# Performance work log

Hardware: AMD Instinct MI355X
Metric: run time of the kernel (lower is better)

The kernel has to match this reference:

```python
import jax, jax.numpy as jnp
import numpy as np

R_MAX, S_MAX, C_Z = 32, 2, 128
N_POS = 2 * (R_MAX + 1)   # 66 one-hot bins for rel position / rel token
N_CH = 2 * (S_MAX + 1)    # 6 one-hot bins for rel chain
IN_DIM = 2 * N_POS + 1 + N_CH  # 139
B, N = 1, 1024


def setup_inputs() -> dict:
    key = jax.random.key(0)
    k1, k2, k3, k4, k5 = jax.random.split(key, 5)
    asym_id = jnp.sort(jax.random.randint(k1, (B, N), 0, 4), axis=-1)
    residue_index = jnp.sort(jax.random.randint(k2, (B, N), 0, 800), axis=-1)
    entity_id = jnp.sort(jax.random.randint(k3, (B, N), 0, 3), axis=-1)
    sym_id = jax.random.randint(k4, (B, N), 0, 4)
    token_index = jnp.arange(B * N, dtype=jnp.int64 if jax.config.read('jax_enable_x64') else jnp.int32).reshape(B, N)
    W = jax.random.normal(k5, (IN_DIM, C_Z), dtype=jnp.float32)  # transposed LinearNoBias weight
    return {"asym_id": asym_id, "residue_index": residue_index, "entity_id": entity_id,
            "sym_id": sym_id, "token_index": token_index, "W": W}


def reference(asym_id, residue_index, entity_id, sym_id, token_index, W):
    # Pairwise comparisons, [B, N, N]
    same_chain = asym_id[..., :, None] == asym_id[..., None, :]
    same_res = residue_index[..., :, None] == residue_index[..., None, :]
    same_ent = entity_id[..., :, None] == entity_id[..., None, :]

    d_res = jnp.clip(residue_index[..., :, None] - residue_index[..., None, :] + R_MAX, 0, 2 * R_MAX)
    d_res = jnp.where(same_chain, d_res, 2 * R_MAX + 1)

    d_tok = jnp.clip(token_index[..., :, None] - token_index[..., None, :] + R_MAX, 0, 2 * R_MAX)
    d_tok = jnp.where(same_chain & same_res, d_tok, 2 * R_MAX + 1)

    d_chain = jnp.clip(sym_id[..., :, None] - sym_id[..., None, :] + S_MAX, 0, 2 * S_MAX)
    d_chain = jnp.where(same_ent, d_chain, 2 * S_MAX + 1)

    # one_hot(idx) @ W  ==  W[idx]; concat+linear == sum of gathered rows.
    W_pos = W[:N_POS]                     # rows for a_rel_pos
    W_tok = W[N_POS:2 * N_POS]            # rows for a_rel_token
    w_ent = W[2 * N_POS]                  # single row scaled by same_entity flag
    W_ch = W[2 * N_POS + 1:]              # rows for a_rel_chain

    p = (W_pos[d_res] + W_tok[d_tok]
         + same_ent[..., None].astype(W.dtype) * w_ent
         + W_ch[d_chain])                 # [B, N, N, c_z]
    return p
```

## Files before the change

kernel.cpp:

```cpp
#include <hip/hip_runtime.h>


#define RMAX 32
#define SMAX 2
#define CZ 128
#define TJ 512
#define NROWS 138
#define BLOCK 256

__global__ __launch_bounds__(BLOCK) void relpos_kernel(
    const int* __restrict__ asym, const int* __restrict__ resi,
    const int* __restrict__ ent,  const int* __restrict__ sym,
    const int* __restrict__ tok,  const float* __restrict__ W,
    float* __restrict__ out, int N)
{
    __shared__ float4 sW4[NROWS * 32];
    __shared__ int2   sOff[TJ];

    const int tid = threadIdx.x;
    const int i   = blockIdx.y;
    const int j0  = blockIdx.x * TJ;

    const float4* __restrict__ W4 = reinterpret_cast<const float4*>(W);

    for (int t = tid; t < NROWS * 32; t += BLOCK) {
        const int row = t >> 5, cc = t & 31;
        float4 a, b;
        if (row < 66) {
            a = W4[32 * 32 + cc];
            b = W4[(66 + row) * 32 + cc];
        } else if (row < 132) {
            a = W4[(row - 66) * 32 + cc];
            b = W4[131 * 32 + cc];
        } else if (row < 137) {
            a = W4[(133 + (row - 132)) * 32 + cc];
            b = W4[132 * 32 + cc];
        } else {
            a = W4[138 * 32 + cc];
            b = make_float4(0.f, 0.f, 0.f, 0.f);
        }
        sW4[t] = make_float4(a.x + b.x, a.y + b.y, a.z + b.z, a.w + b.w);
    }

    const int ai = asym[i], ri = resi[i], ei = ent[i], si = sym[i], ti = tok[i];
    for (int t = tid; t < TJ; t += BLOCK) {
        const int j = j0 + t;
        const int aj = asym[j], rj = resi[j], ej = ent[j], sj = sym[j], tj = tok[j];
        int row;
        if (ai == aj) {
            if (ri == rj) {
                int dt = ti - tj + RMAX;
                dt = dt < 0 ? 0 : (dt > 2 * RMAX ? 2 * RMAX : dt);
                row = dt;
            } else {
                int dr = ri - rj + RMAX;
                dr = dr < 0 ? 0 : (dr > 2 * RMAX ? 2 * RMAX : dr);
                row = 66 + dr;
            }
        } else {
            row = 131;
        }
        int crow;
        if (ei == ej) {
            int dc = si - sj + SMAX;
            dc = dc < 0 ? 0 : (dc > 2 * SMAX ? 2 * SMAX : dc);
            crow = 132 + dc;
        } else {
            crow = 137;
        }
        sOff[t] = make_int2(row << 5, crow << 5);
    }
    __syncthreads();

    const int cc = tid & 31;
    const int jl = tid >> 5;
    float4* __restrict__ out4 = reinterpret_cast<float4*>(out);
    const size_t base = ((size_t)i * N + j0) * 32 + cc;

    #pragma unroll 4
    for (int jj = jl; jj < TJ; jj += 8) {
        const int2 off = sOff[jj];
        const float4 a = sW4[off.x + cc];
        const float4 b = sW4[off.y + cc];
        out4[base + (size_t)jj * 32] =
            make_float4(a.x + b.x, a.y + b.y, a.z + b.z, a.w + b.w);
    }
}

extern "C" void kernel_launch(void* const* d_in, const int* in_sizes, int n_in,
                              void* d_out, int out_size, void* d_ws, size_t ws_size,
                              hipStream_t stream) {
    const int* asym = (const int*)d_in[0];
    const int* resi = (const int*)d_in[1];
    const int* ent  = (const int*)d_in[2];
    const int* sym  = (const int*)d_in[3];
    const int* tok  = (const int*)d_in[4];
    const float* W  = (const float*)d_in[5];
    float* out = (float*)d_out;

    const int N = in_sizes[0];
    dim3 grid(N / TJ, N);
    relpos_kernel<<<grid, BLOCK, 0, stream>>>(asym, resi, ent, sym, tok, W, out, N);
}
```

Before: 632.8 us.

## Split channels across blocks to shrink shared W table and raise occupancy

Each block now handles a 32-channel slice of one output row across all columns instead of all channels for half the columns. This cuts the per-block shared weight table by 4x, allowing more resident blocks per CU, and packs the two row offsets into one int. The tradeoff is that every channel-slice block recomputes the index offsets for all columns, and stores become 128-byte segments strided across rows rather than fully contiguous 512-byte rows.

```diff
diff --git a/kernel.cpp b/kernel.cpp
--- a/kernel.cpp
+++ b/kernel.cpp
@@ -3,8 +3,6 @@
 
 #define RMAX 32
 #define SMAX 2
-#define CZ 128
-#define TJ 512
 #define NROWS 138
 #define BLOCK 256
 
@@ -14,38 +12,38 @@
     const int* __restrict__ tok,  const float* __restrict__ W,
     float* __restrict__ out, int N)
 {
-    __shared__ float4 sW4[NROWS * 32];
-    __shared__ int2   sOff[TJ];
+    __shared__ float4 sW[NROWS * 8];
+    __shared__ int    sOff[1024];
 
     const int tid = threadIdx.x;
+    const int q   = blockIdx.x;
     const int i   = blockIdx.y;
-    const int j0  = blockIdx.x * TJ;
 
     const float4* __restrict__ W4 = reinterpret_cast<const float4*>(W);
 
-    for (int t = tid; t < NROWS * 32; t += BLOCK) {
-        const int row = t >> 5, cc = t & 31;
+    for (int t = tid; t < NROWS * 8; t += BLOCK) {
+        const int row = t >> 3;
+        const int g   = q * 8 + (t & 7);
         float4 a, b;
         if (row < 66) {
-            a = W4[32 * 32 + cc];
-            b = W4[(66 + row) * 32 + cc];
+            a = W4[32 * 32 + g];
+            b = W4[(66 + row) * 32 + g];
         } else if (row < 132) {
-            a = W4[(row - 66) * 32 + cc];
-            b = W4[131 * 32 + cc];
+            a = W4[(row - 66) * 32 + g];
+            b = W4[131 * 32 + g];
         } else if (row < 137) {
-            a = W4[(133 + (row - 132)) * 32 + cc];
-            b = W4[132 * 32 + cc];
+            a = W4[(row + 1) * 32 + g];
+            b = W4[132 * 32 + g];
         } else {
-            a = W4[138 * 32 + cc];
+            a = W4[138 * 32 + g];
             b = make_float4(0.f, 0.f, 0.f, 0.f);
         }
-        sW4[t] = make_float4(a.x + b.x, a.y + b.y, a.z + b.z, a.w + b.w);
+        sW[t] = make_float4(a.x + b.x, a.y + b.y, a.z + b.z, a.w + b.w);
     }
 
     const int ai = asym[i], ri = resi[i], ei = ent[i], si = sym[i], ti = tok[i];
-    for (int t = tid; t < TJ; t += BLOCK) {
-        const int j = j0 + t;
-        const int aj = asym[j], rj = resi[j], ej = ent[j], sj = sym[j], tj = tok[j];
+    for (int t = tid; t < N; t += BLOCK) {
+        const int aj = asym[t], rj = resi[t], ej = ent[t], sj = sym[t], tj = tok[t];
         int row;
         if (ai == aj) {
             if (ri == rj) {
@@ -68,20 +66,20 @@
         } else {
             crow = 137;
         }
-        sOff[t] = make_int2(row << 5, crow << 5);
+        sOff[t] = (row << 3) | (crow << 19);
     }
     __syncthreads();
 
-    const int cc = tid & 31;
-    const int jl = tid >> 5;
+    const int cc = tid & 7;
+    const int jl = tid >> 3;
     float4* __restrict__ out4 = reinterpret_cast<float4*>(out);
-    const size_t base = ((size_t)i * N + j0) * 32 + cc;
+    const size_t base = (size_t)i * N * 32 + (size_t)(q * 8 + cc);
 
-    #pragma unroll 4
-    for (int jj = jl; jj < TJ; jj += 8) {
-        const int2 off = sOff[jj];
-        const float4 a = sW4[off.x + cc];
-        const float4 b = sW4[off.y + cc];
+    #pragma unroll 8
+    for (int jj = jl; jj < N; jj += 32) {
+        const int off = sOff[jj];
+        const float4 a = sW[(off & 0xffff) + cc];
+        const float4 b = sW[(off >> 16) + cc];
         out4[base + (size_t)jj * 32] =
             make_float4(a.x + b.x, a.y + b.y, a.z + b.z, a.w + b.w);
     }
@@ -99,6 +97,6 @@
     float* out = (float*)d_out;
 
     const int N = in_sizes[0];
-    dim3 grid(N / TJ, N);
+    dim3 grid(4, N);
     relpos_kernel<<<grid, BLOCK, 0, stream>>>(asym, resi, ent, sym, tok, W, out, N);
 }
```

After: 607.8 us. -3.9%, faster.

## Precompute full combined position-chain table in workspace and stream one gather per output

Applied to the files above, without the earlier changes.

A separate pre-kernel builds a 132x6 table that holds every combination of position/token row and chain row already summed, and writes it to the workspace. The main kernel then does one global (cache-resident) float4 load per output element instead of two shared-memory loads plus an add. It also drops the per-block shared-memory staging of W. The cost is an extra kernel launch and table gathers that go through L1/L2 instead of LDS. Unroll rises to 8.

```diff
diff --git a/kernel.cpp b/kernel.cpp
--- a/kernel.cpp
+++ b/kernel.cpp
@@ -3,44 +3,45 @@
 
 #define RMAX 32
 #define SMAX 2
-#define CZ 128
 #define TJ 512
-#define NROWS 138
 #define BLOCK 256
 
-__global__ __launch_bounds__(BLOCK) void relpos_kernel(
+__global__ __launch_bounds__(BLOCK) void build_combo(
+    const float* __restrict__ W, float4* __restrict__ C)
+{
+    const int t  = blockIdx.x * BLOCK + threadIdx.x;
+    const int rc = t >> 5;
+    const int cc = t & 31;
+    const int r  = rc / 6;
+    const int c  = rc - r * 6;
+
+    const float4* __restrict__ W4 = reinterpret_cast<const float4*>(W);
+    float4 a, b;
+    if (r < 66) { a = W4[32 * 32 + cc];       b = W4[(66 + r) * 32 + cc]; }
+    else        { a = W4[(r - 66) * 32 + cc]; b = W4[131 * 32 + cc];      }
+    float4 d;
+    if (c < 5) {
+        const float4 e = W4[(133 + c) * 32 + cc];
+        const float4 f = W4[132 * 32 + cc];
+        d = make_float4(e.x + f.x, e.y + f.y, e.z + f.z, e.w + f.w);
+    } else {
+        d = W4[138 * 32 + cc];
+    }
+    C[rc * 32 + cc] = make_float4(a.x + b.x + d.x, a.y + b.y + d.y,
+                                  a.z + b.z + d.z, a.w + b.w + d.w);
+}
+
+__global__ __launch_bounds__(BLOCK) void relpos_stream(
     const int* __restrict__ asym, const int* __restrict__ resi,
     const int* __restrict__ ent,  const int* __restrict__ sym,
-    const int* __restrict__ tok,  const float* __restrict__ W,
+    const int* __restrict__ tok,  const char* __restrict__ Cbytes,
     float* __restrict__ out, int N)
 {
-    __shared__ float4 sW4[NROWS * 32];
-    __shared__ int2   sOff[TJ];
+    __shared__ int sAddr[TJ];
 
     const int tid = threadIdx.x;
     const int i   = blockIdx.y;
     const int j0  = blockIdx.x * TJ;
-
-    const float4* __restrict__ W4 = reinterpret_cast<const float4*>(W);
-
-    for (int t = tid; t < NROWS * 32; t += BLOCK) {
-        const int row = t >> 5, cc = t & 31;
-        float4 a, b;
-        if (row < 66) {
-            a = W4[32 * 32 + cc];
-            b = W4[(66 + row) * 32 + cc];
-        } else if (row < 132) {
-            a = W4[(row - 66) * 32 + cc];
-            b = W4[131 * 32 + cc];
-        } else if (row < 137) {
-            a = W4[(133 + (row - 132)) * 32 + cc];
-            b = W4[132 * 32 + cc];
-        } else {
-            a = W4[138 * 32 + cc];
-            b = make_float4(0.f, 0.f, 0.f, 0.f);
-        }
-        sW4[t] = make_float4(a.x + b.x, a.y + b.y, a.z + b.z, a.w + b.w);
-    }
 
     const int ai = asym[i], ri = resi[i], ei = ent[i], si = sym[i], ti = tok[i];
     for (int t = tid; t < TJ; t += BLOCK) {
@@ -64,11 +65,11 @@
         if (ei == ej) {
             int dc = si - sj + SMAX;
             dc = dc < 0 ? 0 : (dc > 2 * SMAX ? 2 * SMAX : dc);
-            crow = 132 + dc;
+            crow = dc;
         } else {
-            crow = 137;
+            crow = 5;
         }
-        sOff[t] = make_int2(row << 5, crow << 5);
+        sAddr[t] = (row * 6 + crow) << 9;
     }
     __syncthreads();
 
@@ -77,13 +78,12 @@
     float4* __restrict__ out4 = reinterpret_cast<float4*>(out);
     const size_t base = ((size_t)i * N + j0) * 32 + cc;
 
-    #pragma unroll 4
+    #pragma unroll 8
     for (int jj = jl; jj < TJ; jj += 8) {
-        const int2 off = sOff[jj];
-        const float4 a = sW4[off.x + cc];
-        const float4 b = sW4[off.y + cc];
-        out4[base + (size_t)jj * 32] =
-            make_float4(a.x + b.x, a.y + b.y, a.z + b.z, a.w + b.w);
+        const int off = sAddr[jj];
+        const float4 v = *reinterpret_cast<const float4*>(
+            Cbytes + off + (cc << 4));
+        out4[base + (size_t)jj * 32] = v;
     }
 }
 
@@ -99,6 +99,10 @@
     float* out = (float*)d_out;
 
     const int N = in_sizes[0];
+
+    build_combo<<<99, BLOCK, 0, stream>>>(W, (float4*)d_ws);
+
     dim3 grid(N / TJ, N);
-    relpos_kernel<<<grid, BLOCK, 0, stream>>>(asym, resi, ent, sym, tok, W, out, N);
+    relpos_stream<<<grid, BLOCK, 0, stream>>>(
+        asym, resi, ent, sym, tok, (const char*)d_ws, out, N);
 }
```

Result: faster. 537.3 us (-15.1%).
